# Performance work log

Hardware: AMD Instinct MI355X
Metric: run time of the kernel (lower is better)

The kernel has to match this reference:

```python
import jax, jax.numpy as jnp
import numpy as np

N = 50000      # nodes
E = 800000     # edges (avg degree 16)
D = 128        # embed_dim
H = 8          # nhead
HD = D // H    # head dim = 16


def setup_inputs() -> dict:
    key = jax.random.key(0)
    ks = jax.random.split(key, 6)
    s = 1.0 / np.sqrt(D)  # ~xavier scale for square matrices
    return {
        "feats": jax.random.normal(ks[0], (N, D), jnp.float32),
        "edge_index": jax.random.randint(ks[1], (E, 2), 0, N, dtype=jnp.int64),
        "Wq": jax.random.normal(ks[2], (D, D), jnp.float32) * s,
        "bq": jnp.zeros((D,), jnp.float32),
        "Wk": jax.random.normal(ks[3], (D, D), jnp.float32) * s,
        "bk": jnp.zeros((D,), jnp.float32),
        "Wv": jax.random.normal(ks[4], (D, D), jnp.float32) * s,
        "bv": jnp.zeros((D,), jnp.float32),
        "Wo": jax.random.normal(ks[5], (D, D), jnp.float32) * s,
        "bo": jnp.zeros((D,), jnp.float32),
    }


def reference(feats, edge_index, Wq, bq, Wk, bk, Wv, bv, Wo, bo):
    # Projections (nn.Linear: x @ W.T + b), split into heads: [N, H, HD]
    q = (feats @ Wq.T + bq).reshape(N, H, HD)
    k = (feats @ Wk.T + bk).reshape(N, H, HD)
    v = (feats @ Wv.T + bv).reshape(N, H, HD)

    r = edge_index[:, 0]  # source nodes
    c = edge_index[:, 1]  # destination nodes (softmax / aggregation groups)

    # Per-edge, per-head dot-product scores: [E, H]
    scores = jnp.einsum('ehd,ehd->eh', q[c], k[r]) / np.sqrt(HD)

    # Custom scatter-softmax: src_max clamped to min 0; extra exp(-src_max) in denom
    smax = jnp.maximum(jax.ops.segment_max(scores, c, num_segments=N), 0.0)  # [N, H]
    ex = jnp.exp(scores - smax[c])                                           # [E, H]
    denom = jax.ops.segment_sum(ex, c, num_segments=N)                       # [N, H]
    attn = ex / (denom + jnp.exp(-smax))[c]                                  # [E, H]

    # Weighted V per edge, scatter-mean to destination nodes
    out_e = attn[:, :, None] * v[r]                      # [E, H, HD]
    agg = jax.ops.segment_sum(out_e, c, num_segments=N)  # [N, H, HD]
    cnt = jax.ops.segment_sum(jnp.ones((E,), jnp.float32), c, num_segments=N)
    agg = agg / jnp.maximum(cnt, 1.0)[:, None, None]

    return agg.reshape(N, D) @ Wo.T + bo
```

## Files before the change

kernel.cpp:

```cpp
#include <hip/hip_runtime.h>
#include <hip/hip_bf16.h>

#define N_NODES 50000
#define N_EDGES 800000
#define DIM 128
#define NHEAD 8
#define HDIM 16
#define ELL_PAD 64
#define ELL_SLICES 391
#define ELL_BLOCKS (8 * ELL_SLICES)
#define ROWTILES 3125
#define OUT_WAVES (ROWTILES * 2)
#define OUT_GRID ((OUT_WAVES + 3) / 4)
#define AGG_GROUPS 1563
#define AGG_GRID (AGG_GROUPS * 8)

#define Q_OFF      0ull
#define KV_OFF     12800000ull
#define AGG_OFF    38400000ull
#define ELL_OFF    51200000ull
#define CNT_OFF    64000000ull
#define WBF_OFF    64200192ull
#define BIAS_OFF   64331264ull

typedef __attribute__((ext_vector_type(8))) short short8;
typedef __attribute__((ext_vector_type(4))) float floatx4;

__device__ inline float bflo2f(unsigned u) { return __uint_as_float(u << 16); }
__device__ inline float bfhi2f(unsigned u) { return __uint_as_float(u & 0xffff0000u); }
__device__ inline unsigned short f2bf(float f) {
    unsigned u = __float_as_uint(f);
    return (unsigned short)((u + 0x7fffu + ((u >> 16) & 1u)) >> 16);
}

__device__ inline void detect_flags(const void* feats, const void* edge,
                                    int& isbf, int& is32) {
    const unsigned short* f = (const unsigned short*)feats;
    const unsigned int* eg = (const unsigned int*)edge;
    int lane = threadIdx.x & 63;
    unsigned e = (f[lane] >> 7) & 0xFF;
    int junk = (e >= 0x90 || (e > 0 && e <= 0x60)) ? 1 : 0;
    unsigned long long jm = __ballot(junk);
    int nz = (lane < 32 && eg[2 * lane + 1] != 0) ? 1 : 0;
    unsigned long long nm = __ballot(nz);
    isbf = (jm == 0ull) ? 1 : 0;
    is32 = (nm != 0ull) ? 1 : 0;
}

__device__ inline void load_edge(const int* edge, int is32, int e, int& r, int& c) {
    if (is32) { int2 p = ((const int2*)edge)[e]; r = p.x; c = p.y; }
    else {
        const long long* p = (const long long*)edge;
        r = (int)p[2 * e]; c = (int)p[2 * e + 1];
    }
    if ((unsigned)r >= N_NODES) r = 0;
    if ((unsigned)c >= N_NODES) c = 0;
}

__device__ inline float ldf(const void* p, int isbf, int i) {
    return isbf ? __bfloat162float(((const __hip_bfloat16*)p)[i])
                : ((const float*)p)[i];
}

__device__ inline short8 ldfrag(const void* base, int isbf, size_t off) {
    if (isbf) return *(const short8*)((const unsigned short*)base + off);
    const float* f = (const float*)base + off;
    float4 f0 = *(const float4*)f;
    float4 f1 = *(const float4*)(f + 4);
    short8 a;
    a[0] = (short)f2bf(f0.x); a[1] = (short)f2bf(f0.y);
    a[2] = (short)f2bf(f0.z); a[3] = (short)f2bf(f0.w);
    a[4] = (short)f2bf(f1.x); a[5] = (short)f2bf(f1.y);
    a[6] = (short)f2bf(f1.z); a[7] = (short)f2bf(f1.w);
    return a;
}

__global__ __launch_bounds__(256) void ell_build(const void* feats, const int* edge,
                                                 const void* wq, const void* wk,
                                                 const void* wv, const void* wo,
                                                 const void* bq, const void* bk,
                                                 const void* bv, const void* bo,
                                                 int* cnt, int* ell,
                                                 unsigned short* wbf, float* bias) {
    int isbf, is32; detect_flags(feats, edge, isbf, is32);

    if (blockIdx.x >= ELL_BLOCKS) {
        int b2 = blockIdx.x - ELL_BLOCKS;
        if (b2 == 256) {
            for (int j = threadIdx.x; j < 512; j += 256) {
                int m2 = j >> 7;
                const void* bb = (m2 == 0) ? bq : (m2 == 1) ? bk : (m2 == 2) ? bv : bo;
                bias[j] = ldf(bb, isbf, j & 127);
            }
            return;
        }
        if (isbf) return;
        int idx = b2 * 256 + (int)threadIdx.x;
        int mm = idx >> 14, rem = idx & 16383;
        const void* wsrc = (mm == 0) ? wq : (mm == 1) ? wk : (mm == 2) ? wv : wo;
        wbf[idx] = f2bf(((const float*)wsrc)[rem]);
        return;
    }

    int pid = blockIdx.x & 7, slice = blockIdx.x >> 3;
    int base = slice * 2048 + (int)threadIdx.x;
    #pragma unroll
    for (int j = 0; j < 8; ++j) {
        int e = base + j * 256;
        if (e < N_EDGES) {
            int r, c; load_edge(edge, is32, e, r, c);
            if ((c & 7) == pid) {
                int slot = atomicAdd(cnt + c, 1);
                if (slot < ELL_PAD) ell[c * ELL_PAD + slot] = r;
            }
        }
    }
}

__global__ __launch_bounds__(192) void qkv_mfma(const void* feats_raw, const int* edge,
                                                const void* wq_raw, const void* wk_raw,
                                                const void* wv_raw,
                                                const unsigned short* wbf,
                                                const float* bias,
                                                unsigned short* q_s, unsigned short* kv_s) {
    int isbf, is32; detect_flags(feats_raw, edge, isbf, is32);
    int rowtile = blockIdx.x;
    int m = threadIdx.x >> 6;
    int lane = threadIdx.x & 63;
    int mrow = lane & 15, quad = lane >> 4;
    int arow = rowtile * 16 + mrow;

    short8 a[4];
    #pragma unroll
    for (int kt = 0; kt < 4; ++kt)
        a[kt] = ldfrag(feats_raw, isbf, (size_t)arow * DIM + quad * 8 + kt * 32);

    const void* wraw = (m == 0) ? wq_raw : (m == 1) ? wk_raw : wv_raw;
    const unsigned short* wm = isbf ? (const unsigned short*)wraw : wbf + m * 16384;
    int soff = (m == 2) ? 16 : 0;

    for (int nt = 0; nt < 8; ++nt) {
        float b = bias[m * 128 + nt * 16 + mrow];
        floatx4 acc = {b, b, b, b};
        const unsigned short* wp = wm + (size_t)(nt * 16 + mrow) * DIM + quad * 8;
        #pragma unroll
        for (int kt = 0; kt < 4; ++kt) {
            short8 bf = *(const short8*)(wp + kt * 32);
            acc = __builtin_amdgcn_mfma_f32_16x16x32_bf16(a[kt], bf, acc, 0, 0, 0);
        }
        if (m == 0) {
            #pragma unroll
            for (int r4 = 0; r4 < 4; ++r4) {
                int row = rowtile * 16 + quad * 4 + r4;
                q_s[((size_t)nt * N_NODES + row) * 16 + mrow] = f2bf(acc[r4]);
            }
        } else {
            #pragma unroll
            for (int r4 = 0; r4 < 4; ++r4) {
                int row = rowtile * 16 + quad * 4 + r4;
                kv_s[((size_t)nt * N_NODES + row) * 32 + soff + mrow] = f2bf(acc[r4]);
            }
        }
    }
}

__device__ __forceinline__ float dot16(uint4 ka, uint4 kb, const float* qv) {
    float s = 0.f;
    s += bflo2f(ka.x) * qv[0]  + bfhi2f(ka.x) * qv[1];
    s += bflo2f(ka.y) * qv[2]  + bfhi2f(ka.y) * qv[3];
    s += bflo2f(ka.z) * qv[4]  + bfhi2f(ka.z) * qv[5];
    s += bflo2f(ka.w) * qv[6]  + bfhi2f(ka.w) * qv[7];
    s += bflo2f(kb.x) * qv[8]  + bfhi2f(kb.x) * qv[9];
    s += bflo2f(kb.y) * qv[10] + bfhi2f(kb.y) * qv[11];
    s += bflo2f(kb.z) * qv[12] + bfhi2f(kb.z) * qv[13];
    s += bflo2f(kb.w) * qv[14] + bfhi2f(kb.w) * qv[15];
    return s;
}

__device__ __forceinline__ void acc16(float* acc, float p, uint4 va, uint4 vb) {
    acc[0]  += p * bflo2f(va.x); acc[1]  += p * bfhi2f(va.x);
    acc[2]  += p * bflo2f(va.y); acc[3]  += p * bfhi2f(va.y);
    acc[4]  += p * bflo2f(va.z); acc[5]  += p * bfhi2f(va.z);
    acc[6]  += p * bflo2f(va.w); acc[7]  += p * bfhi2f(va.w);
    acc[8]  += p * bflo2f(vb.x); acc[9]  += p * bfhi2f(vb.x);
    acc[10] += p * bflo2f(vb.y); acc[11] += p * bfhi2f(vb.y);
    acc[12] += p * bflo2f(vb.z); acc[13] += p * bfhi2f(vb.z);
    acc[14] += p * bflo2f(vb.w); acc[15] += p * bfhi2f(vb.w);
}

__global__ __launch_bounds__(256) void node_agg(const int* __restrict__ cnt,
                                                const int* __restrict__ ell,
                                                const unsigned short* __restrict__ q_s,
                                                const uint4* __restrict__ kvpack,
                                                uint4* __restrict__ agg_bf) {
    int h = blockIdx.x & 7;
    int grp = blockIdx.x >> 3;
    int w = threadIdx.x >> 6;
    int lane = threadIdx.x & 63;
    int nl = lane >> 3, e = lane & 7;
    int base = grp * 32 + w * 8;
    if (base >= N_NODES) return;
    int node = base + nl;

    const uint4* qp = (const uint4*)((const unsigned short*)q_s
                                     + ((size_t)h * N_NODES + node) * 16);
    uint4 q0 = qp[0], q1 = qp[1];
    float qv[16];
    qv[0]  = bflo2f(q0.x); qv[1]  = bfhi2f(q0.x);
    qv[2]  = bflo2f(q0.y); qv[3]  = bfhi2f(q0.y);
    qv[4]  = bflo2f(q0.z); qv[5]  = bfhi2f(q0.z);
    qv[6]  = bflo2f(q0.w); qv[7]  = bfhi2f(q0.w);
    qv[8]  = bflo2f(q1.x); qv[9]  = bfhi2f(q1.x);
    qv[10] = bflo2f(q1.y); qv[11] = bfhi2f(q1.y);
    qv[12] = bflo2f(q1.z); qv[13] = bfhi2f(q1.z);
    qv[14] = bflo2f(q1.w); qv[15] = bfhi2f(q1.w);

    int degt = cnt[node];
    int deg = degt < ELL_PAD ? degt : ELL_PAD;
    float l = 0.f;
    float acc[16];
    #pragma unroll
    for (int i = 0; i < 16; ++i) acc[i] = 0.f;

    const int* erow = ell + node * ELL_PAD;
    const uint4* kvh = kvpack + (size_t)h * N_NODES * 4;

    for (int i0 = 0; __any(i0 < deg); i0 += 8) {
        int i = i0 + e;
        bool ok = i < deg;
        int r = ok ? erow[i] : 0;
        const uint4* kp = kvh + (size_t)r * 4;
        uint4 ka = kp[0], kb = kp[1], va = kp[2], vb = kp[3];
        float s = dot16(ka, kb, qv);
        float p = ok ? __expf(s * 0.25f) : 0.f;
        l += p;
        acc16(acc, p, va, vb);
    }

    #pragma unroll
    for (int m = 1; m < 8; m <<= 1) {
        l += __shfl_xor(l, m);
        #pragma unroll
        for (int i = 0; i < 16; ++i) acc[i] += __shfl_xor(acc[i], m);
    }

    float inv = 1.0f / ((1.0f + l) * (float)(degt > 0 ? degt : 1));
    if (e == 0) {
        unsigned o[8];
        #pragma unroll
        for (int i = 0; i < 8; ++i)
            o[i] = (unsigned)f2bf(acc[2 * i] * inv) | ((unsigned)f2bf(acc[2 * i + 1] * inv) << 16);
        uint4* op = agg_bf + (size_t)node * 16 + h * 2;
        op[0] = make_uint4(o[0], o[1], o[2], o[3]);
        op[1] = make_uint4(o[4], o[5], o[6], o[7]);
    }
}

__global__ __launch_bounds__(256) void out_mfma(const unsigned short* agg_bf,
                                                const void* feats, const int* edge,
                                                const void* wo_raw,
                                                const unsigned short* wbf,
                                                const float* bias, void* out) {
    int isbf, is32; detect_flags(feats, edge, isbf, is32);
    const unsigned short* W = isbf ? (const unsigned short*)wo_raw : wbf + 3 * 16384;
    int w = blockIdx.x * 4 + (threadIdx.x >> 6);
    if (w >= OUT_WAVES) return;
    int rowtile = w >> 1;
    int nthalf = w & 1;
    int lane = threadIdx.x & 63;
    int mrow = lane & 15, quad = lane >> 4;
    int arow = rowtile * 16 + mrow;

    short8 a[4];
    const unsigned short* ap = agg_bf + (size_t)arow * DIM + quad * 8;
    #pragma unroll
    for (int kt = 0; kt < 4; ++kt) a[kt] = *(const short8*)(ap + kt * 32);

    for (int nt = nthalf * 4; nt < nthalf * 4 + 4; ++nt) {
        float b = bias[3 * 128 + nt * 16 + mrow];
        floatx4 acc = {b, b, b, b};
        const unsigned short* wp = W + (size_t)(nt * 16 + mrow) * DIM + quad * 8;
        #pragma unroll
        for (int kt = 0; kt < 4; ++kt) {
            short8 bf = *(const short8*)(wp + kt * 32);
            acc = __builtin_amdgcn_mfma_f32_16x16x32_bf16(a[kt], bf, acc, 0, 0, 0);
        }
        if (isbf) {
            #pragma unroll
            for (int r4 = 0; r4 < 4; ++r4) {
                int row = rowtile * 16 + quad * 4 + r4;
                ((unsigned short*)out)[(size_t)row * DIM + nt * 16 + mrow] = f2bf(acc[r4]);
            }
        } else {
            #pragma unroll
            for (int r4 = 0; r4 < 4; ++r4) {
                int row = rowtile * 16 + quad * 4 + r4;
                ((float*)out)[(size_t)row * DIM + nt * 16 + mrow] = acc[r4];
            }
        }
    }
}

extern "C" void kernel_launch(void* const* d_in, const int* in_sizes, int n_in,
                              void* d_out, int out_size, void* d_ws, size_t ws_size,
                              hipStream_t stream) {
    const void* feats = d_in[0];
    const int*  edge  = (const int*)d_in[1];
    const void* Wq = d_in[2]; const void* bq = d_in[3];
    const void* Wk = d_in[4]; const void* bk = d_in[5];
    const void* Wv = d_in[6]; const void* bv = d_in[7];
    const void* Wo = d_in[8]; const void* bo = d_in[9];

    char* ws = (char*)d_ws;
    unsigned short* q_s  = (unsigned short*)(ws + Q_OFF);
    unsigned short* kv_s = (unsigned short*)(ws + KV_OFF);
    unsigned short* aggb = (unsigned short*)(ws + AGG_OFF);
    int* ell             = (int*)(ws + ELL_OFF);
    int* cnt             = (int*)(ws + CNT_OFF);
    unsigned short* wbf  = (unsigned short*)(ws + WBF_OFF);
    float* bias          = (float*)(ws + BIAS_OFF);

    hipMemsetAsync(ws + CNT_OFF, 0, N_NODES * 4, stream);

    ell_build<<<ELL_BLOCKS + 257, 256, 0, stream>>>(feats, edge, Wq, Wk, Wv, Wo,
                                                    bq, bk, bv, bo, cnt, ell,
                                                    wbf, bias);

    qkv_mfma<<<ROWTILES, 192, 0, stream>>>(feats, edge, Wq, Wk, Wv, wbf, bias,
                                           q_s, kv_s);

    node_agg<<<AGG_GRID, 256, 0, stream>>>(cnt, ell, q_s,
                                           (const uint4*)(ws + KV_OFF),
                                           (uint4*)aggb);

    out_mfma<<<OUT_GRID, 256, 0, stream>>>(aggb, feats, edge, Wo, wbf, bias, d_out);
}
```

Measured before the change: 262.0 us.

## Split per-edge K/V row across four lanes in node aggregation kernel

Restructures node_agg so that each edge's 64-byte packed K/V record is fetched by four lanes (16 bytes each) instead of one lane loading all four uint4s. Partial dot products are combined with shuffles, the exp weight is shared from K lanes to V lanes, and each wave processes two groups of four nodes with four edge slots per node. This is meant to make gather loads more coalesced and cut per-lane register pressure, at the cost of extra shuffles, redundant exp computation, and half the edge parallelism per node.

```diff
diff --git a/kernel.cpp b/kernel.cpp
--- a/kernel.cpp
+++ b/kernel.cpp
@@ -33,6 +33,13 @@
     return (unsigned short)((u + 0x7fffu + ((u >> 16) & 1u)) >> 16);
 }
 
+__device__ __forceinline__ void ext8(uint4 u, float* f) {
+    f[0] = bflo2f(u.x); f[1] = bfhi2f(u.x);
+    f[2] = bflo2f(u.y); f[3] = bfhi2f(u.y);
+    f[4] = bflo2f(u.z); f[5] = bfhi2f(u.z);
+    f[6] = bflo2f(u.w); f[7] = bfhi2f(u.w);
+}
+
 __device__ inline void detect_flags(const void* feats, const void* edge,
                                     int& isbf, int& is32) {
     const unsigned short* f = (const unsigned short*)feats;
@@ -164,30 +171,6 @@
     }
 }
 
-__device__ __forceinline__ float dot16(uint4 ka, uint4 kb, const float* qv) {
-    float s = 0.f;
-    s += bflo2f(ka.x) * qv[0]  + bfhi2f(ka.x) * qv[1];
-    s += bflo2f(ka.y) * qv[2]  + bfhi2f(ka.y) * qv[3];
-    s += bflo2f(ka.z) * qv[4]  + bfhi2f(ka.z) * qv[5];
-    s += bflo2f(ka.w) * qv[6]  + bfhi2f(ka.w) * qv[7];
-    s += bflo2f(kb.x) * qv[8]  + bfhi2f(kb.x) * qv[9];
-    s += bflo2f(kb.y) * qv[10] + bfhi2f(kb.y) * qv[11];
-    s += bflo2f(kb.z) * qv[12] + bfhi2f(kb.z) * qv[13];
-    s += bflo2f(kb.w) * qv[14] + bfhi2f(kb.w) * qv[15];
-    return s;
-}
-
-__device__ __forceinline__ void acc16(float* acc, float p, uint4 va, uint4 vb) {
-    acc[0]  += p * bflo2f(va.x); acc[1]  += p * bfhi2f(va.x);
-    acc[2]  += p * bflo2f(va.y); acc[3]  += p * bfhi2f(va.y);
-    acc[4]  += p * bflo2f(va.z); acc[5]  += p * bfhi2f(va.z);
-    acc[6]  += p * bflo2f(va.w); acc[7]  += p * bfhi2f(va.w);
-    acc[8]  += p * bflo2f(vb.x); acc[9]  += p * bfhi2f(vb.x);
-    acc[10] += p * bflo2f(vb.y); acc[11] += p * bfhi2f(vb.y);
-    acc[12] += p * bflo2f(vb.z); acc[13] += p * bfhi2f(vb.z);
-    acc[14] += p * bflo2f(vb.w); acc[15] += p * bfhi2f(vb.w);
-}
-
 __global__ __launch_bounds__(256) void node_agg(const int* __restrict__ cnt,
                                                 const int* __restrict__ ell,
                                                 const unsigned short* __restrict__ q_s,
@@ -197,62 +180,64 @@
     int grp = blockIdx.x >> 3;
     int w = threadIdx.x >> 6;
     int lane = threadIdx.x & 63;
-    int nl = lane >> 3, e = lane & 7;
-    int base = grp * 32 + w * 8;
-    if (base >= N_NODES) return;
-    int node = base + nl;
-
-    const uint4* qp = (const uint4*)((const unsigned short*)q_s
-                                     + ((size_t)h * N_NODES + node) * 16);
-    uint4 q0 = qp[0], q1 = qp[1];
-    float qv[16];
-    qv[0]  = bflo2f(q0.x); qv[1]  = bfhi2f(q0.x);
-    qv[2]  = bflo2f(q0.y); qv[3]  = bfhi2f(q0.y);
-    qv[4]  = bflo2f(q0.z); qv[5]  = bfhi2f(q0.z);
-    qv[6]  = bflo2f(q0.w); qv[7]  = bfhi2f(q0.w);
-    qv[8]  = bflo2f(q1.x); qv[9]  = bfhi2f(q1.x);
-    qv[10] = bflo2f(q1.y); qv[11] = bfhi2f(q1.y);
-    qv[12] = bflo2f(q1.z); qv[13] = bfhi2f(q1.z);
-    qv[14] = bflo2f(q1.w); qv[15] = bfhi2f(q1.w);
-
-    int degt = cnt[node];
-    int deg = degt < ELL_PAD ? degt : ELL_PAD;
-    float l = 0.f;
-    float acc[16];
-    #pragma unroll
-    for (int i = 0; i < 16; ++i) acc[i] = 0.f;
-
-    const int* erow = ell + node * ELL_PAD;
-    const uint4* kvh = kvpack + (size_t)h * N_NODES * 4;
-
-    for (int i0 = 0; __any(i0 < deg); i0 += 8) {
-        int i = i0 + e;
-        bool ok = i < deg;
-        int r = ok ? erow[i] : 0;
-        const uint4* kp = kvh + (size_t)r * 4;
-        uint4 ka = kp[0], kb = kp[1], va = kp[2], vb = kp[3];
-        float s = dot16(ka, kb, qv);
-        float p = ok ? __expf(s * 0.25f) : 0.f;
-        l += p;
-        acc16(acc, p, va, vb);
-    }
-
-    #pragma unroll
-    for (int m = 1; m < 8; m <<= 1) {
-        l += __shfl_xor(l, m);
+    int nl = lane >> 4;
+    int slot = (lane >> 2) & 3;
+    int sub = lane & 3;
+
+    const unsigned short* qbase = q_s + (size_t)h * N_NODES * 16;
+    const char* kvb = (const char*)kvpack + (size_t)h * N_NODES * 64;
+
+    for (int g = 0; g < 2; ++g) {
+        int node = grp * 32 + w * 8 + g * 4 + nl;
+        int nodec = node < N_NODES ? node : 0;
+        int degt = node < N_NODES ? cnt[nodec] : 0;
+        int deg = degt < ELL_PAD ? degt : ELL_PAD;
+
+        uint4 qh4 = ((const uint4*)(qbase + (size_t)nodec * 16))[sub & 1];
+        float qh[8]; ext8(qh4, qh);
+
+        float l = 0.f;
+        float acc[8];
         #pragma unroll
-        for (int i = 0; i < 16; ++i) acc[i] += __shfl_xor(acc[i], m);
-    }
-
-    float inv = 1.0f / ((1.0f + l) * (float)(degt > 0 ? degt : 1));
-    if (e == 0) {
-        unsigned o[8];
+        for (int j = 0; j < 8; ++j) acc[j] = 0.f;
+
+        const int* erow = ell + nodec * ELL_PAD;
+        for (int i0 = 0; __any(i0 < deg); i0 += 4) {
+            int i = i0 + slot;
+            bool ok = i < deg;
+            int r = ok ? erow[i] : 0;
+            uint4 kv = *(const uint4*)(kvb + ((size_t)r << 6) + (sub << 4));
+            float v[8]; ext8(kv, v);
+            float d = v[0] * qh[0] + v[1] * qh[1] + v[2] * qh[2] + v[3] * qh[3]
+                    + v[4] * qh[4] + v[5] * qh[5] + v[6] * qh[6] + v[7] * qh[7];
+            float s = d + __shfl_xor(d, 1);
+            float p = __expf(s * 0.25f);
+            float pv = __shfl_xor(p, 2);
+            float pl = (sub & 2) ? pv : p;
+            pl = ok ? pl : 0.f;
+            l += pl;
+            #pragma unroll
+            for (int j = 0; j < 8; ++j) acc[j] += pl * v[j];
+        }
+
         #pragma unroll
-        for (int i = 0; i < 8; ++i)
-            o[i] = (unsigned)f2bf(acc[2 * i] * inv) | ((unsigned)f2bf(acc[2 * i + 1] * inv) << 16);
-        uint4* op = agg_bf + (size_t)node * 16 + h * 2;
-        op[0] = make_uint4(o[0], o[1], o[2], o[3]);
-        op[1] = make_uint4(o[4], o[5], o[6], o[7]);
+        for (int m = 4; m <= 8; m <<= 1) {
+            l += __shfl_xor(l, m);
+            #pragma unroll
+            for (int j = 0; j < 8; ++j) acc[j] += __shfl_xor(acc[j], m);
+        }
+
+        float inv = 1.0f / ((1.0f + l) * (float)(degt > 0 ? degt : 1));
+        if ((lane & 12) == 0 && (sub & 2) && node < N_NODES) {
+            unsigned o[4];
+            #pragma unroll
+            for (int j = 0; j < 4; ++j)
+                o[j] = (unsigned)f2bf(acc[2 * j] * inv)
+                     | ((unsigned)f2bf(acc[2 * j + 1] * inv) << 16);
+            uint4* op = (uint4*)((unsigned short*)agg_bf + (size_t)node * 128 + h * 16)
+                        + (sub & 1);
+            *op = make_uint4(o[0], o[1], o[2], o[3]);
+        }
     }
 }
 
```

Result: slower. 275.4 us (+5.1%).
